# Kernel optimization log

Measured on AMD Instinct MI355X. Metric: run time of the kernel, lower is better.

The kernel has to match this reference:

```python
import jax, jax.numpy as jnp
import numpy as np

B, S, D, H, P = 2, 2048, 1024, 16, 2048  # batch, q_len, d_model, heads, past_len
DEPTH = D // H
W_STD = 0.02


def setup_inputs() -> dict:
    key = jax.random.key(0)
    ks = jax.random.split(key, 5)
    x = jax.random.normal(ks[0], (B, S, D), dtype=jnp.float32)
    past_layer = jax.random.normal(ks[1], (B, 2, H, P, DEPTH), dtype=jnp.float32)
    w_attn = jax.random.normal(ks[2], (D, 3 * D), dtype=jnp.float32) * W_STD
    b_attn = jnp.zeros((3 * D,), dtype=jnp.float32)
    w_proj = jax.random.normal(ks[3], (D, D), dtype=jnp.float32) * W_STD
    b_proj = jnp.zeros((D,), dtype=jnp.float32)
    # causal mask with KV cache: query i sits at absolute position P+i; key j
    # is masked (1.0 -> +(-1e9)) when j > P + i.
    q_pos = P + jnp.arange(S)[:, None]        # [S,1]
    k_pos = jnp.arange(P + S)[None, :]        # [1,P+S]
    mask = (k_pos > q_pos).astype(jnp.float32)[None, None]  # [1,1,S,P+S]
    return {"x": x, "mask": mask, "past_layer": past_layer,
            "w_attn": w_attn, "b_attn": b_attn,
            "w_proj": w_proj, "b_proj": b_proj}


def _split_heads(t):
    # [B,S,D] -> [B,H,S,depth]
    b, s, _ = t.shape
    return t.reshape(b, s, H, DEPTH).transpose(0, 2, 1, 3)


def reference(x, mask, past_layer, w_attn, b_attn, w_proj, b_proj):
    # fused QKV projection (Conv1d == pointwise Linear)
    qkv = jnp.einsum('bsd,de->bse', x, w_attn) + b_attn        # [B,S,3D]
    q, k, v = jnp.split(qkv, 3, axis=2)
    q, k, v = _split_heads(q), _split_heads(k), _split_heads(v)
    # KV-cache concat
    k = jnp.concatenate([past_layer[:, 0], k], axis=2)         # [B,H,P+S,depth]
    v = jnp.concatenate([past_layer[:, 1], v], axis=2)
    present = jnp.stack([k, v], axis=1)                        # [B,2,H,P+S,depth]
    # scaled dot-product attention (full score matrix, eval mode: no dropout)
    scores = jnp.einsum('bhqd,bhkd->bhqk', q, k) / jnp.sqrt(
        jnp.asarray(DEPTH, dtype=jnp.float32))
    scores = scores + mask * (-1e9)
    attn = jax.nn.softmax(scores, axis=-1)
    ctx = jnp.einsum('bhqk,bhkd->bhqd', attn, v)               # [B,H,S,depth]
    merged = ctx.transpose(0, 2, 1, 3).reshape(B, S, D)
    output = jnp.einsum('bsd,de->bse', merged, w_proj) + b_proj
    return output, present
```

## Files before the change

kernel.cpp:

```cpp
#include <hip/hip_runtime.h>
#include <hip/hip_bf16.h>

#define B_ 2
#define S_ 2048
#define D_ 1024
#define H_ 16
#define P_ 2048
#define T_ 4096
#define DEPTH_ 64

typedef __bf16 bf16x8 __attribute__((ext_vector_type(8)));
typedef float  f32x4  __attribute__((ext_vector_type(4)));
typedef short  short8_t __attribute__((ext_vector_type(8)));
typedef unsigned short ushort_t;
typedef unsigned short ushort4_t __attribute__((ext_vector_type(4)));

__device__ __forceinline__ ushort_t f2bf(float f) {
    union { float f; unsigned u; } v; v.f = f;
    return (ushort_t)((v.u + 0x7fffu + ((v.u >> 16) & 1u)) >> 16);
}

__device__ __forceinline__ unsigned cvt_pk_bf16(float lo, float hi) {
    unsigned r;
    asm("v_cvt_pk_bf16_f32 %0, %1, %2" : "=v"(r) : "v"(lo), "v"(hi));
    return r;
}

__device__ __forceinline__ void gload16(const void* g, void* l) {
    __builtin_amdgcn_global_load_lds(
        (const __attribute__((address_space(1))) unsigned int*)g,
        (__attribute__((address_space(3))) unsigned int*)l, 16, 0, 0);
}

__global__ __launch_bounds__(256)
void convert_bf16_kernel(const float4* __restrict__ in, ushort4_t* __restrict__ out, int n4)
{
    for (int i = blockIdx.x * 256 + threadIdx.x; i < n4; i += gridDim.x * 256) {
        float4 v = in[i];
        ushort4_t o;
        o[0] = f2bf(v.x); o[1] = f2bf(v.y); o[2] = f2bf(v.z); o[3] = f2bf(v.w);
        out[i] = o;
    }
}

__global__ __launch_bounds__(256)
void transpose_conv_kernel(const float* __restrict__ w, ushort_t* __restrict__ wt, int N)
{
    __shared__ float t[64][65];
    const int tid = threadIdx.x;
    const int k0 = blockIdx.y * 64, n0 = blockIdx.x * 64;
    #pragma unroll
    for (int rep = 0; rep < 4; ++rep) {
        const int idx = rep * 256 + tid;
        const int r = idx >> 4, c = idx & 15;
        float4 v = *(const float4*)&w[(size_t)(k0 + r) * N + n0 + c * 4];
        t[r][c*4+0] = v.x; t[r][c*4+1] = v.y; t[r][c*4+2] = v.z; t[r][c*4+3] = v.w;
    }
    __syncthreads();
    #pragma unroll
    for (int rep = 0; rep < 4; ++rep) {
        const int idx = rep * 256 + tid;
        const int nl = idx >> 4, kg = idx & 15;
        ushort4_t o;
        o[0] = f2bf(t[kg*4+0][nl]); o[1] = f2bf(t[kg*4+1][nl]);
        o[2] = f2bf(t[kg*4+2][nl]); o[3] = f2bf(t[kg*4+3][nl]);
        *(ushort4_t*)&wt[(size_t)(n0 + nl) * 1024 + k0 + kg*4] = o;
    }
}

template<int MODE>
__global__ __launch_bounds__(256)
void gemm_bf16_kernel(const ushort_t* __restrict__ A,
                      const ushort_t* __restrict__ Bt,
                      const float*  __restrict__ bias,
                      ushort_t* __restrict__ out_qb,
                      float*  __restrict__ out_present,
                      float*  __restrict__ out_plain)
{
    __shared__ __attribute__((aligned(16))) ushort_t As[128*32];
    __shared__ __attribute__((aligned(16))) ushort_t Bs[128*32];

    const int tid  = threadIdx.x;
    const int w    = tid >> 6;
    const int lane = tid & 63;
    const int g    = lane >> 4;
    const int ln   = lane & 15;
    const int wr   = w >> 1, wc = w & 1;
    const int row0 = blockIdx.y * 128;
    const int col0 = blockIdx.x * 128;

    int srow[2], sgl[2];
    #pragma unroll
    for (int r = 0; r < 2; ++r) {
        const int o = (w*2 + r) * 1024 + lane * 16;
        srow[r] = o >> 6;
        const int gp = (o >> 4) & 3;
        sgl[r] = gp ^ ((srow[r] >> 1) & 3);
    }

    f32x4 acc[4][4];
    #pragma unroll
    for (int i = 0; i < 4; ++i)
        #pragma unroll
        for (int j = 0; j < 4; ++j)
            acc[i][j] = (f32x4){0.f, 0.f, 0.f, 0.f};

    for (int k0 = 0; k0 < 1024; k0 += 32) {
        #pragma unroll
        for (int r = 0; r < 2; ++r) {
            const int lb = (w*2 + r) * 512;
            gload16(&A [(size_t)(row0 + srow[r]) * 1024 + k0 + sgl[r]*8], &As[lb]);
            gload16(&Bt[(size_t)(col0 + srow[r]) * 1024 + k0 + sgl[r]*8], &Bs[lb]);
        }
        __syncthreads();

        bf16x8 af[4], bfr[4];
        #pragma unroll
        for (int i = 0; i < 4; ++i) {
            const int ra = wr*64 + i*16 + ln;
            const int ga = g ^ ((ra >> 1) & 3);
            af[i] = __builtin_bit_cast(bf16x8, *(const short8_t*)&As[ra*32 + ga*8]);
            const int rb = wc*64 + i*16 + ln;
            const int gb = g ^ ((rb >> 1) & 3);
            bfr[i] = __builtin_bit_cast(bf16x8, *(const short8_t*)&Bs[rb*32 + gb*8]);
        }
        #pragma unroll
        for (int i = 0; i < 4; ++i)
            #pragma unroll
            for (int j = 0; j < 4; ++j)
                acc[i][j] = __builtin_amdgcn_mfma_f32_16x16x32_bf16(af[i], bfr[j], acc[i][j], 0, 0, 0);
        __syncthreads();
    }

    #pragma unroll
    for (int i = 0; i < 4; ++i) {
        #pragma unroll
        for (int j = 0; j < 4; ++j) {
            const int rm = row0 + wr*64 + i*16 + g*4 + j;
            const int b  = rm >> 11;
            const int s  = rm & 2047;
            #pragma unroll
            for (int jn = 0; jn < 4; ++jn) {
                const int e = col0 + wc*64 + jn*16 + ln;
                const float v = acc[i][jn][j] + bias[e];
                if (MODE == 0) {
                    const int which = e >> 10;
                    const int f = e & 1023;
                    const int h = f >> 6, d = f & 63;
                    if (which == 0) {
                        out_qb[(size_t)(((b*16 + h) * 2048 + s) << 6) + d] =
                            f2bf(v * 0.18033688f);
                    } else {
                        const int kv = which - 1;
                        out_present[((((size_t)(b*2 + kv)*16 + h) * 4096 + 2048 + s) << 6) + d] = v;
                    }
                } else {
                    out_plain[(size_t)rm * 1024 + e] = v;
                }
            }
        }
    }
}

__global__ __launch_bounds__(256)
void prep_kv_kernel(const float* __restrict__ past,
                    float* __restrict__ present,
                    ushort_t* __restrict__ Kws, ushort_t* __restrict__ Vws)
{
    __shared__ float tv[64][65];
    const int tid = threadIdx.x;
    const int kt  = blockIdx.x;
    const int bh  = blockIdx.y;
    const int b   = bh >> 4, h = bh & 15;
    const bool old = (kt < 32);

    const float* Kp = old ? past    + (((size_t)(b*2+0)*16 + h) * P_ + kt*64) * 64
                          : present + (((size_t)(b*2+0)*16 + h) * T_ + kt*64) * 64;
    const float* Vp = old ? past    + (((size_t)(b*2+1)*16 + h) * P_ + kt*64) * 64
                          : present + (((size_t)(b*2+1)*16 + h) * T_ + kt*64) * 64;
    float4* PKo = (float4*)(present + (((size_t)(b*2+0)*16 + h) * T_ + kt*64) * 64);
    float4* PVo = (float4*)(present + (((size_t)(b*2+1)*16 + h) * T_ + kt*64) * 64);
    ushort_t* Kd = Kws + ((size_t)bh * T_ + kt*64) * 64;

    #pragma unroll
    for (int rep = 0; rep < 4; ++rep) {
        const int idx = rep * 256 + tid;
        float4 v = ((const float4*)Kp)[idx];
        if (old) PKo[idx] = v;
        ushort4_t o;
        o[0] = f2bf(v.x); o[1] = f2bf(v.y); o[2] = f2bf(v.z); o[3] = f2bf(v.w);
        *(ushort4_t*)&Kd[idx*4] = o;
        float4 vv = ((const float4*)Vp)[idx];
        if (old) PVo[idx] = vv;
        const int r = idx >> 4, c = idx & 15;
        tv[r][c*4+0] = vv.x; tv[r][c*4+1] = vv.y;
        tv[r][c*4+2] = vv.z; tv[r][c*4+3] = vv.w;
    }
    __syncthreads();
    #pragma unroll
    for (int rep = 0; rep < 4; ++rep) {
        const int idx = rep * 256 + tid;
        const int d = idx >> 4, pg = idx & 15;
        ushort4_t o;
        o[0] = f2bf(tv[pg*4+0][d]); o[1] = f2bf(tv[pg*4+1][d]);
        o[2] = f2bf(tv[pg*4+2][d]); o[3] = f2bf(tv[pg*4+3][d]);
        *(ushort4_t*)&Vws[((size_t)bh*64 + d) * T_ + kt*64 + pg*4] = o;
    }
}

__global__ __launch_bounds__(256, 4)
void attn_v8_kernel(const ushort_t* __restrict__ qin,
                    const ushort_t* __restrict__ Kws,
                    const ushort_t* __restrict__ Vws,
                    ushort_t* __restrict__ merged)
{
    __shared__ __attribute__((aligned(16))) ushort_t Kb0[4096];
    __shared__ __attribute__((aligned(16))) ushort_t Kb1[4096];
    __shared__ __attribute__((aligned(16))) ushort_t Vb0[4096];
    __shared__ __attribute__((aligned(16))) ushort_t Vb1[4096];

    const int tid  = threadIdx.x;
    const int w    = tid >> 6;
    const int lane = tid & 63;
    const int g    = lane >> 4;
    const int ln   = lane & 15;
    const int lnm  = ln & 7;
    const int lsub = lane >> 3;
    const int swz8 = ((lane & 7) ^ lsub) * 8;

    const int bid = (int)blockIdx.x;
    const int a   = bid & 7;
    const int m_c = (bid >> 3) & 31;
    const int j   = bid >> 8;
    const int bh  = a * 4 + (m_c & 3);
    const int c   = m_c >> 2;
    const int qblk = (j == 0) ? c : (j == 1) ? (15 - c) : (j == 2) ? (16 + c) : (31 - c);
    const int q0   = qblk * 64;
    const int b    = bh >> 4, h = bh & 15;

    const ushort_t* Kbase = Kws + (size_t)bh * T_ * 64;
    const ushort_t* Vbase = Vws + (size_t)bh * 64 * T_;
    const int nt = 33 + qblk;

    const int kgOff0 = ((w*16 + 0 + lsub) << 6) + swz8;
    const int kgOff1 = ((w*16 + 8 + lsub) << 6) + swz8;
    const size_t vgOff0 = (size_t)(w*16 + 0 + lsub) * T_ + swz8;
    const size_t vgOff1 = (size_t)(w*16 + 8 + lsub) * T_ + swz8;
    const int ldsOff0 = (w*2 + 0) * 512;
    const int ldsOff1 = (w*2 + 1) * 512;
    const int pRow = (w*16 + ln) * 64;

    gload16(Kbase + kgOff0, &Kb0[ldsOff0]);
    gload16(Kbase + kgOff1, &Kb0[ldsOff1]);
    gload16(Vbase + vgOff0, &Vb0[ldsOff0]);
    gload16(Vbase + vgOff1, &Vb0[ldsOff1]);

    bf16x8 qf[2];
    {
        const ushort_t* Qr = qin + ((size_t)bh * S_ + q0 + w*16 + ln) * 64;
        #pragma unroll
        for (int kh = 0; kh < 2; ++kh)
            qf[kh] = __builtin_bit_cast(bf16x8, *(const short8_t*)(Qr + kh*32 + g*8));
    }

    f32x4 o[4];
    #pragma unroll
    for (int d = 0; d < 4; ++d) o[d] = (f32x4){0.f, 0.f, 0.f, 0.f};
    float m = -3.0e38f, l = 0.f;

#define ATTN_BODY(KBUF, VBUF, NBUF_K, NBUF_V)                                   \
    {                                                                           \
        asm volatile("s_waitcnt vmcnt(0)" ::: "memory");                        \
        __builtin_amdgcn_s_barrier();                                           \
        __builtin_amdgcn_sched_barrier(0);                                      \
        if (t + 1 < nt) {                                                       \
            const size_t t0n = (size_t)(t + 1) * 64;                            \
            gload16(Kbase + (t0n << 6) + kgOff0, &NBUF_K[ldsOff0]);             \
            gload16(Kbase + (t0n << 6) + kgOff1, &NBUF_K[ldsOff1]);             \
            gload16(Vbase + vgOff0 + t0n, &NBUF_V[ldsOff0]);                    \
            gload16(Vbase + vgOff1 + t0n, &NBUF_V[ldsOff1]);                    \
            __builtin_amdgcn_sched_barrier(0);                                  \
        }                                                                       \
        f32x4 st[4];                                                            \
        __builtin_amdgcn_s_setprio(1);                                          \
        _Pragma("unroll")                                                       \
        for (int js = 0; js < 4; ++js) {                                        \
            const ushort_t* kr = &KBUF[(js*16 + ln) * 64];                      \
            bf16x8 a0 = __builtin_bit_cast(bf16x8, *(const short8_t*)(kr + ((    g) ^ lnm)*8)); \
            bf16x8 a1 = __builtin_bit_cast(bf16x8, *(const short8_t*)(kr + ((4 + g) ^ lnm)*8)); \
            f32x4 z = (f32x4){0.f, 0.f, 0.f, 0.f};                              \
            z = __builtin_amdgcn_mfma_f32_16x16x32_bf16(a0, qf[0], z, 0, 0, 0); \
            z = __builtin_amdgcn_mfma_f32_16x16x32_bf16(a1, qf[1], z, 0, 0, 0); \
            st[js] = z;                                                         \
        }                                                                       \
        __builtin_amdgcn_s_setprio(0);                                          \
        if (t == nt - 1) {                                                      \
            const int qr = w*16 + ln;                                           \
            _Pragma("unroll")                                                   \
            for (int js = 0; js < 4; ++js)                                      \
                _Pragma("unroll")                                               \
                for (int r = 0; r < 4; ++r)                                     \
                    if (js*16 + g*4 + r > qr) st[js][r] = -1e30f;               \
        }                                                                       \
        float mj[4];                                                            \
        _Pragma("unroll")                                                       \
        for (int js = 0; js < 4; ++js)                                          \
            mj[js] = fmaxf(fmaxf(st[js][0], st[js][1]), fmaxf(st[js][2], st[js][3])); \
        float mx = fmaxf(fmaxf(mj[0], mj[1]), fmaxf(mj[2], mj[3]));             \
        mx = fmaxf(mx, __shfl_xor(mx, 16));                                     \
        mx = fmaxf(mx, __shfl_xor(mx, 32));                                     \
        if (!__all(mx <= m + 8.0f)) {                                           \
            const float mnew = fmaxf(m, mx);                                    \
            const float corr = exp2f(m - mnew);                                 \
            m = mnew;                                                           \
            l *= corr;                                                          \
            _Pragma("unroll")                                                   \
            for (int d = 0; d < 4; ++d)                                         \
                _Pragma("unroll")                                               \
                for (int r = 0; r < 4; ++r)                                     \
                    o[d][r] *= corr;                                            \
        }                                                                       \
          \
        __builtin_amdgcn_s_barrier();                                           \
        float rs = 0.f;                                                         \
        _Pragma("unroll")                                                       \
        for (int js = 0; js < 4; ++js) {                                        \
            float p0 = exp2f(st[js][0] - m);                                    \
            float p1 = exp2f(st[js][1] - m);                                    \
            float p2 = exp2f(st[js][2] - m);                                    \
            float p3 = exp2f(st[js][3] - m);                                    \
            rs += (p0 + p1) + (p2 + p3);                                        \
            uint2 pk;                                                           \
            pk.x = cvt_pk_bf16(p0, p1);                                         \
            pk.y = cvt_pk_bf16(p2, p3);                                         \
            *(uint2*)&KBUF[pRow + (((js*4 + g) ^ (lnm << 1)) << 2)] = pk;       \
        }                                                                       \
        rs += __shfl_xor(rs, 16);                                               \
        rs += __shfl_xor(rs, 32);                                               \
        l += rs;                                                                \
        __builtin_amdgcn_s_setprio(1);                                          \
        _Pragma("unroll")                                                       \
        for (int kh = 0; kh < 2; ++kh) {                                        \
            bf16x8 pfr = __builtin_bit_cast(bf16x8,                             \
                           *(const short8_t*)&KBUF[pRow + (((kh*4 + g) ^ lnm) << 3)]); \
            _Pragma("unroll")                                                   \
            for (int dsub = 0; dsub < 4; ++dsub) {                              \
                const ushort_t* vr = &VBUF[(dsub*16 + ln) * 64];                \
                bf16x8 va = __builtin_bit_cast(bf16x8,                          \
                              *(const short8_t*)(vr + ((kh*4 + g) ^ lnm)*8));   \
                o[dsub] = __builtin_amdgcn_mfma_f32_16x16x32_bf16(va, pfr, o[dsub], 0, 0, 0); \
            }                                                                   \
        }                                                                       \
        __builtin_amdgcn_s_setprio(0);                                          \
    }

    int t = 0;
    for (;;) {
        ATTN_BODY(Kb0, Vb0, Kb1, Vb1);
        if (++t == nt) break;
        ATTN_BODY(Kb1, Vb1, Kb0, Vb0);
        if (++t == nt) break;
    }
#undef ATTN_BODY

    const float inv = 1.f / l;
    const int row = q0 + w*16 + ln;
    #pragma unroll
    for (int dsub = 0; dsub < 4; ++dsub) {
        ushort4_t ov;
        ov[0] = f2bf(o[dsub][0] * inv);
        ov[1] = f2bf(o[dsub][1] * inv);
        ov[2] = f2bf(o[dsub][2] * inv);
        ov[3] = f2bf(o[dsub][3] * inv);
        *(ushort4_t*)&merged[((size_t)b * S_ + row) * D_ + h*64 + dsub*16 + g*4] = ov;
    }
}

extern "C" void kernel_launch(void* const* d_in, const int* in_sizes, int n_in,
                              void* d_out, int out_size, void* d_ws, size_t ws_size,
                              hipStream_t stream)
{
    const float* x      = (const float*)d_in[0];
    const float* past   = (const float*)d_in[2];
    const float* w_attn = (const float*)d_in[3];
    const float* b_attn = (const float*)d_in[4];
    const float* w_proj = (const float*)d_in[5];
    const float* b_proj = (const float*)d_in[6];

    float* out     = (float*)d_out;
    float* present = out + (size_t)B_ * S_ * D_;

    ushort_t* wsu     = (ushort_t*)d_ws;
    ushort_t* q_ws    = wsu;
    ushort_t* mergedb = wsu + 4194304;
    ushort_t* wptb    = wsu + 8388608;
    ushort_t* xb      = wsu + 9437184;
    ushort_t* watb    = wsu + 13631488;
    ushort_t* K_ws    = wsu + 9437184;
    ushort_t* V_ws    = wsu + 17825792;

    convert_bf16_kernel<<<2048, 256, 0, stream>>>(
        (const float4*)x, (ushort4_t*)xb, (B_*S_*D_)/4);
    transpose_conv_kernel<<<dim3(48, 16), 256, 0, stream>>>(w_attn, watb, 3072);
    transpose_conv_kernel<<<dim3(16, 16), 256, 0, stream>>>(w_proj, wptb, 1024);

    gemm_bf16_kernel<0><<<dim3(24, 32), 256, 0, stream>>>(
        xb, watb, b_attn, q_ws, present, nullptr);

    prep_kv_kernel<<<dim3(64, 32), 256, 0, stream>>>(past, present, K_ws, V_ws);

    attn_v8_kernel<<<dim3(1024), 256, 0, stream>>>(q_ws, K_ws, V_ws, mergedb);

    gemm_bf16_kernel<1><<<dim3(8, 32), 256, 0, stream>>>(
        mergedb, wptb, b_proj, nullptr, nullptr, out);
}
```

Baseline: 207.0 us.

## Split K/V load waits and defer row-sum reduction in attention loop

The single vmcnt(0) wait at the top of each tile becomes two partial waits. K is waited for before QK^T, and V is waited for later, before the P·V stage, so the V load can overlap the score and max computation. The cross-lane max shuffle now runs only when a rescale is needed, and the per-lane row-sum shuffles move out of the loop into one final reduction. The vmcnt counts depend on the order of the issued loads, and the conditional shuffle inside __all assumes the row max stays consistent across lane groups, which carries a correctness risk.

```diff
diff --git a/kernel.cpp b/kernel.cpp
--- a/kernel.cpp
+++ b/kernel.cpp
@@ -209,7 +209,7 @@
 }
 
 __global__ __launch_bounds__(256, 4)
-void attn_v8_kernel(const ushort_t* __restrict__ qin,
+void attn_v9_kernel(const ushort_t* __restrict__ qin,
                     const ushort_t* __restrict__ Kws,
                     const ushort_t* __restrict__ Vws,
                     ushort_t* __restrict__ merged)
@@ -270,10 +270,12 @@
 
 #define ATTN_BODY(KBUF, VBUF, NBUF_K, NBUF_V)                                   \
     {                                                                           \
-        asm volatile("s_waitcnt vmcnt(0)" ::: "memory");                        \
+                    \
+        asm volatile("s_waitcnt vmcnt(2)" ::: "memory");                        \
         __builtin_amdgcn_s_barrier();                                           \
         __builtin_amdgcn_sched_barrier(0);                                      \
-        if (t + 1 < nt) {                                                       \
+        const bool haspf = (t + 1 < nt);                                        \
+        if (haspf) {                                                            \
             const size_t t0n = (size_t)(t + 1) * 64;                            \
             gload16(Kbase + (t0n << 6) + kgOff0, &NBUF_K[ldsOff0]);             \
             gload16(Kbase + (t0n << 6) + kgOff1, &NBUF_K[ldsOff1]);             \
@@ -302,15 +304,18 @@
                 for (int r = 0; r < 4; ++r)                                     \
                     if (js*16 + g*4 + r > qr) st[js][r] = -1e30f;               \
         }                                                                       \
+                  \
         float mj[4];                                                            \
         _Pragma("unroll")                                                       \
-        for (int js = 0; js < 4; ++js)                                          \
-            mj[js] = fmaxf(fmaxf(st[js][0], st[js][1]), fmaxf(st[js][2], st[js][3])); \
-        float mx = fmaxf(fmaxf(mj[0], mj[1]), fmaxf(mj[2], mj[3]));             \
-        mx = fmaxf(mx, __shfl_xor(mx, 16));                                     \
-        mx = fmaxf(mx, __shfl_xor(mx, 32));                                     \
-        if (!__all(mx <= m + 8.0f)) {                                           \
-            const float mnew = fmaxf(m, mx);                                    \
+        for (int js = 0; js < 4; ++js) {                                        \
+            float m01 = fmaxf(st[js][0], st[js][1]);                            \
+            mj[js] = fmaxf(fmaxf(m01, st[js][2]), st[js][3]);                   \
+        }                                                                       \
+        float mx16 = fmaxf(fmaxf(fmaxf(mj[0], mj[1]), mj[2]), mj[3]);           \
+        if (!__all(mx16 <= m + 8.0f)) {                                         \
+            float gmx = fmaxf(mx16, __shfl_xor(mx16, 16));                      \
+            gmx = fmaxf(gmx, __shfl_xor(gmx, 32));                              \
+            const float mnew = fmaxf(m, gmx);                                   \
             const float corr = exp2f(m - mnew);                                 \
             m = mnew;                                                           \
             l *= corr;                                                          \
@@ -320,8 +325,11 @@
                 for (int r = 0; r < 4; ++r)                                     \
                     o[d][r] *= corr;                                            \
         }                                                                       \
-          \
+            \
+        if (haspf) { asm volatile("s_waitcnt vmcnt(4)" ::: "memory"); }         \
+        else       { asm volatile("s_waitcnt vmcnt(0)" ::: "memory"); }         \
         __builtin_amdgcn_s_barrier();                                           \
+        __builtin_amdgcn_sched_barrier(0);                                      \
         float rs = 0.f;                                                         \
         _Pragma("unroll")                                                       \
         for (int js = 0; js < 4; ++js) {                                        \
@@ -335,8 +343,6 @@
             pk.y = cvt_pk_bf16(p2, p3);                                         \
             *(uint2*)&KBUF[pRow + (((js*4 + g) ^ (lnm << 1)) << 2)] = pk;       \
         }                                                                       \
-        rs += __shfl_xor(rs, 16);                                               \
-        rs += __shfl_xor(rs, 32);                                               \
         l += rs;                                                                \
         __builtin_amdgcn_s_setprio(1);                                          \
         _Pragma("unroll")                                                       \
@@ -363,7 +369,9 @@
     }
 #undef ATTN_BODY
 
-    const float inv = 1.f / l;
+    float lf = l + __shfl_xor(l, 16);
+    lf = lf + __shfl_xor(lf, 32);
+    const float inv = 1.f / lf;
     const int row = q0 + w*16 + ln;
     #pragma unroll
     for (int dsub = 0; dsub < 4; ++dsub) {
@@ -409,7 +417,7 @@
 
     prep_kv_kernel<<<dim3(64, 32), 256, 0, stream>>>(past, present, K_ws, V_ws);
 
-    attn_v8_kernel<<<dim3(1024), 256, 0, stream>>>(q_ws, K_ws, V_ws, mergedb);
+    attn_v9_kernel<<<dim3(1024), 256, 0, stream>>>(q_ws, K_ws, V_ws, mergedb);
 
     gemm_bf16_kernel<1><<<dim3(8, 32), 256, 0, stream>>>(
         mergedb, wptb, b_proj, nullptr, nullptr, out);
```

New measurement: 200.9 us. -2.9%, faster.
